# Performance work log

Measured on AMD Instinct MI355X. Metric: run time of the kernel, lower is better.

The kernel has to match this reference:

```python
import jax, jax.numpy as jnp
import numpy as np
import math

NUM_HEADS = 8

def setup_inputs() -> dict:
    key = jax.random.key(0)
    ks = jax.random.split(key, 5)
    b, h, w, c = 4, 128, 128, 256
    x = jax.random.normal(ks[0], (b, h, w, c), dtype=jnp.float32)
    scale = 1.0 / math.sqrt(c)  # keep weights reasonably scaled (kaiming-like)
    Wq = jax.random.normal(ks[1], (c, c), dtype=jnp.float32) * scale
    Wk = jax.random.normal(ks[2], (c, c), dtype=jnp.float32) * scale
    Wv = jax.random.normal(ks[3], (c, c), dtype=jnp.float32) * scale
    Wout = jax.random.normal(ks[4], (c, c), dtype=jnp.float32) * scale
    return {"x": x, "Wq": Wq, "Wk": Wk, "Wv": Wv, "Wout": Wout}

def reference(x, Wq, Wk, Wv, Wout):
    b, h, w, c = x.shape
    hw = h * w
    heads = NUM_HEADS
    dh = c // heads
    xs = x.reshape(b, hw, c)
    q = xs @ Wq  # (b, hw, c)
    k = xs @ Wk
    v = xs @ Wv

    def split_heads(t):
        # (b, hw, c) -> (b, c, hw) -> (b, heads, dh, hw)
        return t.transpose(0, 2, 1).reshape(b, heads, dh, hw)

    q = split_heads(q)
    k = split_heads(k)
    v = split_heads(v)
    # L2-normalize along the feature (hw) axis; original has no epsilon
    q = q / jnp.linalg.norm(q, axis=-1, keepdims=True)
    k = k / jnp.linalg.norm(k, axis=-1, keepdims=True)
    d_k = q.shape[-1]  # = hw
    attn = jnp.einsum('bhcd,bhed->bhce', q, k) / math.sqrt(d_k)  # (b,heads,dh,dh)
    attn = jax.nn.softmax(attn, axis=-1)
    vals = jnp.einsum('bhce,bhed->bhcd', attn, v)  # (b,heads,dh,hw)
    vals = vals.transpose(0, 3, 1, 2).reshape(b, hw, c)
    out = (vals @ Wout).reshape(b, h, w, c)
    return out
```

## Files before the change

### kernel.cpp

```cpp
#include <hip/hip_runtime.h>


#define B_   4
#define HW_  16384
#define C_   256

typedef __attribute__((ext_vector_type(8))) short short8;
typedef __attribute__((ext_vector_type(4))) float floatx4;

__device__ __forceinline__ unsigned short f2bf(float f) {
  unsigned u = __builtin_bit_cast(unsigned, f);
  u += 0x7FFFu + ((u >> 16) & 1u);
  return (unsigned short)(u >> 16);
}

__device__ __forceinline__ void gl_lds16(const unsigned short* g, unsigned short* l) {
  __builtin_amdgcn_global_load_lds(
      (const __attribute__((address_space(1))) unsigned int*)g,
      (__attribute__((address_space(3))) unsigned int*)l, 16, 0, 0);
}

__global__ __launch_bounds__(256) void k_cast_tr(const float* __restrict__ x,
                                                 unsigned short* __restrict__ xb,
                                                 unsigned short* __restrict__ xT) {
  __shared__ unsigned short lds[64][72];
  int bid = blockIdx.x;
  int t = threadIdx.x;
  int ct = bid & 3;
  int pt = (bid >> 2) & 255;
  int b  = bid >> 10;
  const float* src = x + ((size_t)(b * HW_ + pt * 64)) * C_ + ct * 64;
#pragma unroll
  for (int e = 0; e < 4; e++) {
    int lin = t + e * 256;
    int p = lin >> 4, c4 = lin & 15;
    float4 v = *(const float4*)(src + (size_t)p * C_ + c4 * 4);
    ushort4 h;
    h.x = f2bf(v.x); h.y = f2bf(v.y); h.z = f2bf(v.z); h.w = f2bf(v.w);
    *(ushort4*)(xb + ((size_t)(b * HW_ + pt * 64 + p)) * C_ + ct * 64 + c4 * 4) = h;
    lds[c4 * 4 + 0][p] = h.x;
    lds[c4 * 4 + 1][p] = h.y;
    lds[c4 * 4 + 2][p] = h.z;
    lds[c4 * 4 + 3][p] = h.w;
  }
  __syncthreads();
#pragma unroll
  for (int e = 0; e < 4; e++) {
    int lin = t + e * 256;
    int c = lin >> 4, p4 = lin & 15;
    ushort4 h;
    h.x = lds[c][p4 * 4 + 0];
    h.y = lds[c][p4 * 4 + 1];
    h.z = lds[c][p4 * 4 + 2];
    h.w = lds[c][p4 * 4 + 3];
    *(ushort4*)(xT + ((size_t)(b * C_ + ct * 64 + c)) * HW_ + pt * 64 + p4 * 4) = h;
  }
}

__global__ __launch_bounds__(512) void k_sgemm(const unsigned short* __restrict__ xT,
                                               float* __restrict__ part) {
  __shared__ unsigned short Pt[256 * 128];
  int bid = blockIdx.x;
  int ks = bid & 31, b = bid >> 5;
  const unsigned short* Pb = xT + ((size_t)b * C_) * HW_ + ks * 512;
  int t = threadIdx.x, lane = t & 63, w = t >> 6;
  int wq = w >> 1, h = w & 1;
  int wm = wq >> 1, wn = wq & 1;
  int l15 = lane & 15, l4 = lane >> 4;
  floatx4 acc[4][8];
  floatx4 z = {0.f, 0.f, 0.f, 0.f};
#pragma unroll
  for (int i = 0; i < 4; i++)
#pragma unroll
    for (int j = 0; j < 8; j++) acc[i][j] = z;

  for (int ph = 0; ph < 4; ph++) {
    if (ph) __syncthreads();
#pragma unroll
    for (int i = 0; i < 8; i++) {
      int issue = w * 8 + i;
      int row = issue * 4 + l4;
      int goct = l15 ^ (row & 15);
      gl_lds16(Pb + (size_t)row * HW_ + ph * 128 + goct * 8, Pt + issue * 512);
    }
    __syncthreads();
#pragma unroll
    for (int kk = 0; kk < 4; kk++) {
      short8 af[4], bfv[8];
      int oct = kk * 4 + l4;
#pragma unroll
      for (int tm = 0; tm < 4; tm++) {
        int row = wm * 128 + h * 64 + tm * 16 + l15;
        af[tm] = *(const short8*)(Pt + row * 128 + ((oct ^ (row & 15)) * 8));
      }
#pragma unroll
      for (int tn = 0; tn < 8; tn++) {
        int row = wn * 128 + tn * 16 + l15;
        bfv[tn] = *(const short8*)(Pt + row * 128 + ((oct ^ (row & 15)) * 8));
      }
#pragma unroll
      for (int tm = 0; tm < 4; tm++)
#pragma unroll
        for (int tn = 0; tn < 8; tn++)
          acc[tm][tn] = __builtin_amdgcn_mfma_f32_16x16x32_bf16(af[tm], bfv[tn],
                                                                acc[tm][tn], 0, 0, 0);
    }
  }
  float* pb = part + (size_t)(b * 32 + ks) * 65536;
#pragma unroll
  for (int tm = 0; tm < 4; tm++)
#pragma unroll
    for (int tn = 0; tn < 8; tn++)
#pragma unroll
      for (int r = 0; r < 4; r++) {
        int m = wm * 128 + h * 64 + tm * 16 + l4 * 4 + r;
        int n = wn * 128 + tn * 16 + l15;
        pb[m * 256 + n] = acc[tm][tn][r];
      }
}

__global__ __launch_bounds__(256) void k_sred(const float* __restrict__ part,
                                              float* __restrict__ S) {
  int idx = blockIdx.x * 256 + threadIdx.x;
  int b = idx >> 16;
  int mn = idx & 65535;
  const float* p = part + ((size_t)b << 21) + mn;
  float s = 0.f;
#pragma unroll
  for (int k = 0; k < 32; k++) s += p[(size_t)k << 16];
  S[idx] = s;
}

__global__ __launch_bounds__(256) void k_gemm_sw(const float* __restrict__ S,
                                                 const float* __restrict__ Wq,
                                                 const float* __restrict__ Wk,
                                                 float* __restrict__ SWq,
                                                 float* __restrict__ SWk) {
  __shared__ float Ast[16][68];
  __shared__ float Bs[16][68];
  int bid = blockIdx.x;
  int nt = bid & 7, mt = (bid >> 3) & 3, b = bid >> 5;
  int mb = mt * 64;
  const float* Wsel = (nt < 4) ? Wq : Wk;
  int nb = (nt & 3) * 64;
  int t = threadIdx.x, tx = t & 15, ty = t >> 4;
  float acc[4][4] = {};
  for (int kt = 0; kt < 16; kt++) {
    {
      int row = t >> 2, kq = t & 3;
      float4 v = *(const float4*)(S + ((size_t)(b * C_ + mb + row)) * C_ + kt * 16 + kq * 4);
      Ast[kq * 4 + 0][row] = v.x; Ast[kq * 4 + 1][row] = v.y;
      Ast[kq * 4 + 2][row] = v.z; Ast[kq * 4 + 3][row] = v.w;
    }
    {
      int kk = t >> 4, n4 = t & 15;
      float4 v = *(const float4*)(Wsel + ((size_t)(kt * 16 + kk)) * C_ + nb + n4 * 4);
      *(float4*)&Bs[kk][n4 * 4] = v;
    }
    __syncthreads();
#pragma unroll
    for (int k = 0; k < 16; k++) {
      float4 a4 = *(const float4*)&Ast[k][ty * 4];
      float4 b4 = *(const float4*)&Bs[k][tx * 4];
      float a[4] = {a4.x, a4.y, a4.z, a4.w};
      float bb[4] = {b4.x, b4.y, b4.z, b4.w};
#pragma unroll
      for (int i = 0; i < 4; i++)
#pragma unroll
        for (int j = 0; j < 4; j++) acc[i][j] += a[i] * bb[j];
    }
    __syncthreads();
  }
#pragma unroll
  for (int i = 0; i < 4; i++)
#pragma unroll
    for (int j = 0; j < 4; j++) {
      int row = mb + ty * 4 + i;
      int ng = nt * 64 + tx * 4 + j;
      if (ng < 256) SWq[((size_t)(b * C_ + row)) * C_ + ng] = acc[i][j];
      else          SWk[((size_t)(b * C_ + row)) * C_ + ng - 256] = acc[i][j];
    }
}

__global__ __launch_bounds__(256) void k_fuse(const float* __restrict__ Wq,
                                              const float* __restrict__ Wk,
                                              const float* __restrict__ SWq,
                                              const float* __restrict__ SWk,
                                              const float* __restrict__ Wout,
                                              float* __restrict__ U) {
  __shared__ float Wqh[256][32];
  __shared__ float Wkh[256][32];
  __shared__ float SWqh[256][32];
  __shared__ float SWkh[256][32];
  __shared__ float Lg[32][33];
  __shared__ float qp[8][32], kp[8][32], qin[32], kin[32];
  int b = blockIdx.x >> 3, h = blockIdx.x & 7;
  int t = threadIdx.x;
  int col = t & 31, rgrp = t >> 5;
  for (int r0 = 0; r0 < 256; r0 += 8) {
    int row = r0 + rgrp;
    Wqh[row][col]  = Wq[(size_t)row * C_ + h * 32 + col];
    Wkh[row][col]  = Wk[(size_t)row * C_ + h * 32 + col];
    SWqh[row][col] = SWq[((size_t)(b * C_ + row)) * C_ + h * 32 + col];
    SWkh[row][col] = SWk[((size_t)(b * C_ + row)) * C_ + h * 32 + col];
  }
  __syncthreads();
  {
    float g[4] = {0.f, 0.f, 0.f, 0.f};
    for (int k = 0; k < 256; k++) {
      float swk = SWkh[k][col];
#pragma unroll
      for (int r = 0; r < 4; r++) g[r] += Wqh[k][rgrp + 8 * r] * swk;
    }
#pragma unroll
    for (int r = 0; r < 4; r++) Lg[rgrp + 8 * r][col] = g[r];
  }
  {
    float sq = 0.f, sk = 0.f;
    for (int k = rgrp * 32; k < rgrp * 32 + 32; k++) {
      sq += Wqh[k][col] * SWqh[k][col];
      sk += Wkh[k][col] * SWkh[k][col];
    }
    qp[rgrp][col] = sq;
    kp[rgrp][col] = sk;
  }
  __syncthreads();
  if (t < 32) {
    float a = 0.f;
#pragma unroll
    for (int p = 0; p < 8; p++) a += qp[p][t];
    qin[t] = rsqrtf(a);
  } else if (t < 64) {
    int j = t - 32;
    float a = 0.f;
#pragma unroll
    for (int p = 0; p < 8; p++) a += kp[p][j];
    kin[j] = rsqrtf(a);
  }
  __syncthreads();
  if (t < 32) {
    float row[32];
    float mx = -1e30f;
#pragma unroll
    for (int j = 0; j < 32; j++) {
      row[j] = Lg[t][j] * qin[t] * kin[j] * 0.0078125f;
      mx = fmaxf(mx, row[j]);
    }
    float sum = 0.f;
#pragma unroll
    for (int j = 0; j < 32; j++) { row[j] = __expf(row[j] - mx); sum += row[j]; }
    float inv = 1.0f / sum;
#pragma unroll
    for (int j = 0; j < 32; j++) Lg[t][j] = row[j] * inv;
  }
  __syncthreads();
  float (*Wo)[256] = reinterpret_cast<float(*)[256]>(&Wqh[0][0]);
#pragma unroll
  for (int r = 0; r < 32; r++) Wo[r][t] = Wout[((size_t)(h * 32 + r)) * C_ + t];
  __syncthreads();
  for (int j = 0; j < 32; j++) {
    float a = 0.f;
#pragma unroll
    for (int i2 = 0; i2 < 32; i2++) a += Lg[i2][j] * Wo[i2][t];
    U[((size_t)(b * C_ + h * 32 + j)) * C_ + t] = a;
  }
}

__global__ __launch_bounds__(256) void k_gemm_w3(const float* __restrict__ Wv,
                                                 const float* __restrict__ U,
                                                 unsigned short* __restrict__ W3bT) {
  __shared__ float Ast[16][68];
  __shared__ float Bs[16][68];
  int bid = blockIdx.x;
  int nt = bid & 3, mt = (bid >> 2) & 3, b = bid >> 4;
  int mb = mt * 64, nb = nt * 64;
  int t = threadIdx.x, tx = t & 15, ty = t >> 4;
  float acc[4][4] = {};
  for (int kt = 0; kt < 16; kt++) {
    {
      int row = t >> 2, kq = t & 3;
      float4 v = *(const float4*)(Wv + ((size_t)(mb + row)) * C_ + kt * 16 + kq * 4);
      Ast[kq * 4 + 0][row] = v.x; Ast[kq * 4 + 1][row] = v.y;
      Ast[kq * 4 + 2][row] = v.z; Ast[kq * 4 + 3][row] = v.w;
    }
    {
      int kk = t >> 4, n4 = t & 15;
      float4 v = *(const float4*)(U + ((size_t)(b * C_ + kt * 16 + kk)) * C_ + nb + n4 * 4);
      *(float4*)&Bs[kk][n4 * 4] = v;
    }
    __syncthreads();
#pragma unroll
    for (int k = 0; k < 16; k++) {
      float4 a4 = *(const float4*)&Ast[k][ty * 4];
      float4 b4 = *(const float4*)&Bs[k][tx * 4];
      float a[4] = {a4.x, a4.y, a4.z, a4.w};
      float bb[4] = {b4.x, b4.y, b4.z, b4.w};
#pragma unroll
      for (int i = 0; i < 4; i++)
#pragma unroll
        for (int j = 0; j < 4; j++) acc[i][j] += a[i] * bb[j];
    }
    __syncthreads();
  }
#pragma unroll
  for (int i = 0; i < 4; i++)
#pragma unroll
    for (int j = 0; j < 4; j++)
      W3bT[((size_t)(b * C_ + nb + tx * 4 + j)) * C_ + mb + ty * 4 + i] = f2bf(acc[i][j]);
}

__global__ __launch_bounds__(256) void k_out(const unsigned short* __restrict__ xb,
                                             const unsigned short* __restrict__ W3bT,
                                             float* __restrict__ out) {
  __shared__ unsigned short At[128 * 64];
  __shared__ unsigned short Bt[256 * 64];
  int mtile = blockIdx.x;
  int b = mtile >> 7;
  const unsigned short* Ab = xb + (size_t)mtile * 128 * C_;
  const unsigned short* Bb = W3bT + (size_t)b * C_ * C_;
  int t = threadIdx.x, lane = t & 63, w = t >> 6;
  int h = w >> 1, c2 = w & 1;
  int l8 = lane >> 3, l7 = lane & 7;
  int srcoct = l7 ^ l8;
  int l15 = lane & 15, l4 = lane >> 4;
  floatx4 acc[4][8];
  floatx4 z = {0.f, 0.f, 0.f, 0.f};
#pragma unroll
  for (int i = 0; i < 4; i++)
#pragma unroll
    for (int j = 0; j < 8; j++) acc[i][j] = z;
  for (int s = 0; s < 4; s++) {
    if (s) __syncthreads();
#pragma unroll
    for (int i = 0; i < 4; i++) {
      int ia = w * 4 + i;
      int row = ia * 8 + l8;
      gl_lds16(Ab + (size_t)row * C_ + s * 64 + srcoct * 8, At + ia * 512);
    }
#pragma unroll
    for (int i = 0; i < 8; i++) {
      int ib = w * 8 + i;
      int row = ib * 8 + l8;
      gl_lds16(Bb + (size_t)row * C_ + s * 64 + srcoct * 8, Bt + ib * 512);
    }
    __syncthreads();
#pragma unroll
    for (int kk = 0; kk < 2; kk++) {
      short8 af[4], bfv[8];
      int oct = kk * 4 + l4;
#pragma unroll
      for (int tm = 0; tm < 4; tm++) {
        int row = h * 64 + tm * 16 + l15;
        af[tm] = *(const short8*)(At + row * 64 + ((oct ^ (row & 7)) * 8));
      }
#pragma unroll
      for (int tn = 0; tn < 8; tn++) {
        int row = c2 * 128 + tn * 16 + l15;
        bfv[tn] = *(const short8*)(Bt + row * 64 + ((oct ^ (row & 7)) * 8));
      }
#pragma unroll
      for (int tm = 0; tm < 4; tm++)
#pragma unroll
        for (int tn = 0; tn < 8; tn++)
          acc[tm][tn] = __builtin_amdgcn_mfma_f32_16x16x32_bf16(af[tm], bfv[tn],
                                                                acc[tm][tn], 0, 0, 0);
    }
  }
  float* ob = out + (size_t)mtile * 128 * C_;
#pragma unroll
  for (int tm = 0; tm < 4; tm++)
#pragma unroll
    for (int tn = 0; tn < 8; tn++)
#pragma unroll
      for (int r = 0; r < 4; r++) {
        int m = h * 64 + tm * 16 + l4 * 4 + r;
        int n = c2 * 128 + tn * 16 + l15;
        ob[(size_t)m * C_ + n] = acc[tm][tn][r];
      }
}

extern "C" void kernel_launch(void* const* d_in, const int* in_sizes, int n_in,
                              void* d_out, int out_size, void* d_ws, size_t ws_size,
                              hipStream_t stream) {
  const float* x    = (const float*)d_in[0];
  const float* Wq   = (const float*)d_in[1];
  const float* Wk   = (const float*)d_in[2];
  const float* Wv   = (const float*)d_in[3];
  const float* Wout = (const float*)d_in[4];
  float* out = (float*)d_out;

  unsigned short* xT = (unsigned short*)d_ws;
  unsigned short* xb = xT + (size_t)16777216;
  float* part = (float*)(xb + (size_t)16777216);
  float* S    = part + (size_t)8388608;
  float* SWq  = S + 262144;
  float* SWk  = SWq + 262144;
  float* U    = SWk + 262144;
  unsigned short* W3bT = (unsigned short*)(U + 262144);

  k_cast_tr<<<dim3(4096), dim3(256), 0, stream>>>(x, xb, xT);
  k_sgemm<<<dim3(128), dim3(512), 0, stream>>>(xT, part);
  k_sred<<<dim3(1024), dim3(256), 0, stream>>>(part, S);
  k_gemm_sw<<<dim3(128), dim3(256), 0, stream>>>(S, Wq, Wk, SWq, SWk);
  k_fuse<<<dim3(32), dim3(256), 0, stream>>>(Wq, Wk, SWq, SWk, Wout, U);
  k_gemm_w3<<<dim3(64), dim3(256), 0, stream>>>(Wv, U, W3bT);
  k_out<<<dim3(512), dim3(256), 0, stream>>>(xb, W3bT, out);
}
```

Baseline: 232.0 us.

## Fuse fp32-to-bf16 cast and transpose into Gram and output GEMM kernels

Measured after the change: 218.9 us. -5.6%, faster.

```diff
diff --git a/kernel.cpp b/kernel.cpp
--- a/kernel.cpp
+++ b/kernel.cpp
@@ -20,53 +20,18 @@
       (__attribute__((address_space(3))) unsigned int*)l, 16, 0, 0);
 }
 
-__global__ __launch_bounds__(256) void k_cast_tr(const float* __restrict__ x,
-                                                 unsigned short* __restrict__ xb,
-                                                 unsigned short* __restrict__ xT) {
-  __shared__ unsigned short lds[64][72];
-  int bid = blockIdx.x;
-  int t = threadIdx.x;
-  int ct = bid & 3;
-  int pt = (bid >> 2) & 255;
-  int b  = bid >> 10;
-  const float* src = x + ((size_t)(b * HW_ + pt * 64)) * C_ + ct * 64;
-#pragma unroll
-  for (int e = 0; e < 4; e++) {
-    int lin = t + e * 256;
-    int p = lin >> 4, c4 = lin & 15;
-    float4 v = *(const float4*)(src + (size_t)p * C_ + c4 * 4);
-    ushort4 h;
-    h.x = f2bf(v.x); h.y = f2bf(v.y); h.z = f2bf(v.z); h.w = f2bf(v.w);
-    *(ushort4*)(xb + ((size_t)(b * HW_ + pt * 64 + p)) * C_ + ct * 64 + c4 * 4) = h;
-    lds[c4 * 4 + 0][p] = h.x;
-    lds[c4 * 4 + 1][p] = h.y;
-    lds[c4 * 4 + 2][p] = h.z;
-    lds[c4 * 4 + 3][p] = h.w;
-  }
-  __syncthreads();
-#pragma unroll
-  for (int e = 0; e < 4; e++) {
-    int lin = t + e * 256;
-    int c = lin >> 4, p4 = lin & 15;
-    ushort4 h;
-    h.x = lds[c][p4 * 4 + 0];
-    h.y = lds[c][p4 * 4 + 1];
-    h.z = lds[c][p4 * 4 + 2];
-    h.w = lds[c][p4 * 4 + 3];
-    *(ushort4*)(xT + ((size_t)(b * C_ + ct * 64 + c)) * HW_ + pt * 64 + p4 * 4) = h;
-  }
-}
-
-__global__ __launch_bounds__(512) void k_sgemm(const unsigned short* __restrict__ xT,
+__global__ __launch_bounds__(512) void k_sgemm(const float* __restrict__ x,
                                                float* __restrict__ part) {
   __shared__ unsigned short Pt[256 * 128];
   int bid = blockIdx.x;
   int ks = bid & 31, b = bid >> 5;
-  const unsigned short* Pb = xT + ((size_t)b * C_) * HW_ + ks * 512;
+  const float* xv = x + ((size_t)(b * HW_ + ks * 512)) * C_;
   int t = threadIdx.x, lane = t & 63, w = t >> 6;
-  int wq = w >> 1, h = w & 1;
+  int wq = w >> 1, hh = w & 1;
   int wm = wq >> 1, wn = wq & 1;
   int l15 = lane & 15, l4 = lane >> 4;
+  int s_cq  = (lane >> 3) | (w << 3);
+  int s_hpl = lane & 7;
   floatx4 acc[4][8];
   floatx4 z = {0.f, 0.f, 0.f, 0.f};
 #pragma unroll
@@ -77,11 +42,21 @@
   for (int ph = 0; ph < 4; ph++) {
     if (ph) __syncthreads();
 #pragma unroll
-    for (int i = 0; i < 8; i++) {
-      int issue = w * 8 + i;
-      int row = issue * 4 + l4;
-      int goct = l15 ^ (row & 15);
-      gl_lds16(Pb + (size_t)row * HW_ + ph * 128 + goct * 8, Pt + issue * 512);
+    for (int e = 0; e < 8; e++) {
+      int hp = s_hpl | (e << 3);
+      int hw = hp * 2;
+      const float* src = xv + ((size_t)(ph * 128 + hw)) * C_ + s_cq * 4;
+      float4 v0 = *(const float4*)src;
+      float4 v1 = *(const float4*)(src + C_);
+      float a0[4] = {v0.x, v0.y, v0.z, v0.w};
+      float a1[4] = {v1.x, v1.y, v1.z, v1.w};
+#pragma unroll
+      for (int i = 0; i < 4; i++) {
+        unsigned u = (unsigned)f2bf(a0[i]) | ((unsigned)f2bf(a1[i]) << 16);
+        int r = s_cq * 4 + i;
+        int slot = (hp >> 2) ^ (r & 15);
+        ((unsigned*)Pt)[r * 64 + slot * 4 + (hp & 3)] = u;
+      }
     }
     __syncthreads();
 #pragma unroll
@@ -90,7 +65,7 @@
       int oct = kk * 4 + l4;
 #pragma unroll
       for (int tm = 0; tm < 4; tm++) {
-        int row = wm * 128 + h * 64 + tm * 16 + l15;
+        int row = wm * 128 + hh * 64 + tm * 16 + l15;
         af[tm] = *(const short8*)(Pt + row * 128 + ((oct ^ (row & 15)) * 8));
       }
 #pragma unroll
@@ -113,7 +88,7 @@
     for (int tn = 0; tn < 8; tn++)
 #pragma unroll
       for (int r = 0; r < 4; r++) {
-        int m = wm * 128 + h * 64 + tm * 16 + l4 * 4 + r;
+        int m = wm * 128 + hh * 64 + tm * 16 + l4 * 4 + r;
         int n = wn * 128 + tn * 16 + l15;
         pb[m * 256 + n] = acc[tm][tn][r];
       }
@@ -309,17 +284,16 @@
       W3bT[((size_t)(b * C_ + nb + tx * 4 + j)) * C_ + mb + ty * 4 + i] = f2bf(acc[i][j]);
 }
 
-__global__ __launch_bounds__(256) void k_out(const unsigned short* __restrict__ xb,
+__global__ __launch_bounds__(256) void k_out(const float* __restrict__ x,
                                              const unsigned short* __restrict__ W3bT,
                                              float* __restrict__ out) {
-  __shared__ unsigned short At[128 * 64];
   __shared__ unsigned short Bt[256 * 64];
   int mtile = blockIdx.x;
   int b = mtile >> 7;
-  const unsigned short* Ab = xb + (size_t)mtile * 128 * C_;
+  const float* Ax = x + (size_t)mtile * 128 * C_;
   const unsigned short* Bb = W3bT + (size_t)b * C_ * C_;
   int t = threadIdx.x, lane = t & 63, w = t >> 6;
-  int h = w >> 1, c2 = w & 1;
+  int hf = w >> 1, c2 = w & 1;
   int l8 = lane >> 3, l7 = lane & 7;
   int srcoct = l7 ^ l8;
   int l15 = lane & 15, l4 = lane >> 4;
@@ -332,12 +306,6 @@
   for (int s = 0; s < 4; s++) {
     if (s) __syncthreads();
 #pragma unroll
-    for (int i = 0; i < 4; i++) {
-      int ia = w * 4 + i;
-      int row = ia * 8 + l8;
-      gl_lds16(Ab + (size_t)row * C_ + s * 64 + srcoct * 8, At + ia * 512);
-    }
-#pragma unroll
     for (int i = 0; i < 8; i++) {
       int ib = w * 8 + i;
       int row = ib * 8 + l8;
@@ -350,8 +318,16 @@
       int oct = kk * 4 + l4;
 #pragma unroll
       for (int tm = 0; tm < 4; tm++) {
-        int row = h * 64 + tm * 16 + l15;
-        af[tm] = *(const short8*)(At + row * 64 + ((oct ^ (row & 7)) * 8));
+        int row = hf * 64 + tm * 16 + l15;
+        const float* p = Ax + (size_t)row * C_ + s * 64 + oct * 8;
+        float4 u0 = *(const float4*)p;
+        float4 u1 = *(const float4*)(p + 4);
+        short8 v;
+        v[0] = (short)f2bf(u0.x); v[1] = (short)f2bf(u0.y);
+        v[2] = (short)f2bf(u0.z); v[3] = (short)f2bf(u0.w);
+        v[4] = (short)f2bf(u1.x); v[5] = (short)f2bf(u1.y);
+        v[6] = (short)f2bf(u1.z); v[7] = (short)f2bf(u1.w);
+        af[tm] = v;
       }
 #pragma unroll
       for (int tn = 0; tn < 8; tn++) {
@@ -373,7 +349,7 @@
     for (int tn = 0; tn < 8; tn++)
 #pragma unroll
       for (int r = 0; r < 4; r++) {
-        int m = h * 64 + tm * 16 + l4 * 4 + r;
+        int m = hf * 64 + tm * 16 + l4 * 4 + r;
         int n = c2 * 128 + tn * 16 + l15;
         ob[(size_t)m * C_ + n] = acc[tm][tn][r];
       }
@@ -389,20 +365,17 @@
   const float* Wout = (const float*)d_in[4];
   float* out = (float*)d_out;
 
-  unsigned short* xT = (unsigned short*)d_ws;
-  unsigned short* xb = xT + (size_t)16777216;
-  float* part = (float*)(xb + (size_t)16777216);
+  float* part = (float*)d_ws;
   float* S    = part + (size_t)8388608;
   float* SWq  = S + 262144;
   float* SWk  = SWq + 262144;
   float* U    = SWk + 262144;
   unsigned short* W3bT = (unsigned short*)(U + 262144);
 
-  k_cast_tr<<<dim3(4096), dim3(256), 0, stream>>>(x, xb, xT);
-  k_sgemm<<<dim3(128), dim3(512), 0, stream>>>(xT, part);
+  k_sgemm<<<dim3(128), dim3(512), 0, stream>>>(x, part);
   k_sred<<<dim3(1024), dim3(256), 0, stream>>>(part, S);
   k_gemm_sw<<<dim3(128), dim3(256), 0, stream>>>(S, Wq, Wk, SWq, SWk);
   k_fuse<<<dim3(32), dim3(256), 0, stream>>>(Wq, Wk, SWq, SWk, Wout, U);
   k_gemm_w3<<<dim3(64), dim3(256), 0, stream>>>(Wv, U, W3bT);
-  k_out<<<dim3(512), dim3(256), 0, stream>>>(xb, W3bT, out);
-}
+  k_out<<<dim3(512), dim3(256), 0, stream>>>(x, W3bT, out);
+}
```
